# Performance work log

Measured on AMD Instinct MI355X. Metric: run time of the kernel, lower is better.

## Reference

```python
import jax, jax.numpy as jnp
import numpy as np

HID = 1024
BATCH = 32
SRC = 2048

def setup_inputs() -> dict:
    key = jax.random.key(0)
    k1, k2, k3, k4, k5 = jax.random.split(key, 5)
    hidden = jax.random.normal(k1, (BATCH, HID), dtype=jnp.float32)
    encoder_outputs = jax.random.normal(k2, (BATCH, SRC, HID), dtype=jnp.float32)
    # nn.Linear(2H, H): weight [H, 2H], bias [H]
    lim = 1.0 / np.sqrt(2 * HID)
    attn_w = jax.random.uniform(k3, (HID, 2 * HID), dtype=jnp.float32, minval=-lim, maxval=lim)
    attn_b = jax.random.uniform(k4, (HID,), dtype=jnp.float32, minval=-lim, maxval=lim)
    v = jax.random.uniform(k5, (HID,), dtype=jnp.float32)  # torch.rand
    return {"hidden": hidden, "encoder_outputs": encoder_outputs,
            "attn_w": attn_w, "attn_b": attn_b, "v": v}

def reference(hidden, encoder_outputs, attn_w, attn_b, v):
    # Split the concat linear: cat([hidden, enc]) @ W^T == hidden @ Wh^T + enc @ We^T
    w_h = attn_w[:, :HID]          # [H, H] acts on repeated hidden
    w_e = attn_w[:, HID:]          # [H, H] acts on encoder outputs
    # energy: [B, S, H]
    energy = jnp.tanh(
        jnp.einsum('bh,oh->bo', hidden, w_h)[:, None, :]
        + jnp.einsum('bsh,oh->bso', encoder_outputs, w_e)
        + attn_b
    )
    scores = jnp.einsum('bso,o->bs', energy, v)  # [B, S]
    return jax.nn.softmax(scores, axis=1)
```

## Files before the change

### kernel.cpp

```cpp
#include <hip/hip_runtime.h>
#include <hip/hip_bf16.h>

#define HID    1024
#define NBATCH 32
#define SRC    2048
#define MROWS  (NBATCH * SRC)

typedef _Float16 f16;
typedef f16   f16x8 __attribute__((ext_vector_type(8)));
typedef f16   f16x4 __attribute__((ext_vector_type(4)));
typedef float f32x4 __attribute__((ext_vector_type(4)));

#define BAR()    asm volatile("s_barrier" ::: "memory")
#define VMCNT(n) asm volatile("s_waitcnt vmcnt(" #n ")" ::: "memory")

__device__ __forceinline__ void gload_lds16(const void* g, void* l) {
  __builtin_amdgcn_global_load_lds(
      (const __attribute__((address_space(1))) void*)g,
      (__attribute__((address_space(3))) void*)l, 16, 0, 0);
}

__device__ __forceinline__ float fast_tanh(float x) {
  x = fminf(fmaxf(x, -15.f), 15.f);
  float e = __expf(2.f * x);
  return (e - 1.f) / (e + 1.f);
}

__global__ void convw_k(const float* __restrict__ attn_w, f16* __restrict__ Wf) {
  int idx = blockIdx.x * 256 + threadIdx.x;
  int j = idx * 4;
  int o = j >> 10, h = j & 1023;
  f32x4 d = *(const f32x4*)(attn_w + (size_t)o * 2048 + HID + h);
  f16x4 q = { (f16)d[0], (f16)d[1], (f16)d[2], (f16)d[3] };
  *(f16x4*)(Wf + (size_t)o * HID + h) = q;
}

__global__ void hvec_k(const float* __restrict__ hidden,
                       const float* __restrict__ attn_w,
                       const float* __restrict__ attn_b,
                       float* __restrict__ hvec) {
  int idx = blockIdx.x * 256 + threadIdx.x;
  int b = idx >> 10, o = idx & 1023;
  const float* wrow = attn_w + (size_t)o * 2048;
  const float* hrow = hidden + (size_t)b * HID;
  float acc = 0.f;
  for (int h = 0; h < HID; h += 4) {
    f32x4 wv = *(const f32x4*)(wrow + h);
    f32x4 hv = *(const f32x4*)(hrow + h);
    acc += wv[0]*hv[0] + wv[1]*hv[1] + wv[2]*hv[2] + wv[3]*hv[3];
  }
  hvec[idx] = acc + attn_b[o];
}

__global__ void convA_k(const float* __restrict__ A, f16* __restrict__ Af) {
  size_t i = ((size_t)blockIdx.x * 256 + threadIdx.x) * 8;
  f32x4 d0 = *(const f32x4*)(A + i);
  f32x4 d1 = *(const f32x4*)(A + i + 4);
  f16x8 q = { (f16)d0[0], (f16)d0[1], (f16)d0[2], (f16)d0[3],
              (f16)d1[0], (f16)d1[1], (f16)d1[2], (f16)d1[3] };
  *(f16x8*)(Af + i) = q;
}


#define STG(T) do { \
  char* la_ = lds + ((T) % 3) * 49152; char* lb_ = la_ + 32768; \
  _Pragma("unroll") for (int i_ = 0; i_ < 4; ++i_) \
    gload_lds16(Ab + (size_t)(i_ * 64 + w * 8 + sr8) * HID + (T) * 64 + scol, \
                la_ + i_ * 8192 + w * 1024); \
  _Pragma("unroll") for (int i_ = 0; i_ < 2; ++i_) \
    gload_lds16(Bb + (size_t)(i_ * 64 + w * 8 + sr8) * HID + (T) * 64 + scol, \
                lb_ + i_ * 8192 + w * 1024); } while (0)

__global__ __launch_bounds__(512, 2) void gemm_f16(
    const f16*  __restrict__ Af,
    const f16*  __restrict__ Wf,
    const float* __restrict__ hvec,
    const float* __restrict__ v,
    float* __restrict__ part)
{
  extern __shared__ __align__(16) char lds[];

  int bid = blockIdx.x;
  int wg = (bid & 7) * 256 + (bid >> 3);
  int m_idx = wg >> 3, n_idx = wg & 7;
  long row0 = (long)m_idx * 256;
  int o0 = n_idx * 128;
  int b = (int)(row0 >> 11);

  int tid = threadIdx.x;
  int l = tid & 63, w = tid >> 6;
  int wr = w >> 2, wc = w & 3;
  int lr = l & 15, lg = l >> 4;
  int sr8 = l >> 3;
  int scol = ((l & 7) ^ sr8) << 3;
  int sw = (lr & 7) << 3;

  const f16* Ab = Af + row0 * HID;
  const f16* Bb = Wf + (size_t)o0 * HID;

  f32x4 acc[8][2];
#pragma unroll
  for (int m = 0; m < 8; ++m) {
    acc[m][0] = (f32x4){0.f, 0.f, 0.f, 0.f};
    acc[m][1] = (f32x4){0.f, 0.f, 0.f, 0.f};
  }

  STG(0); STG(1);
  VMCNT(6); BAR();

  for (int T = 0; T < 16; ++T) {
    if (T + 2 < 16) STG(T + 2);
    const char* la = lds + (T % 3) * 49152;
    const char* lb = la + 32768;

    f16x8 bF[2][2];
#pragma unroll
    for (int n = 0; n < 2; ++n)
#pragma unroll
      for (int ks = 0; ks < 2; ++ks)
        bF[n][ks] = *(const f16x8*)(lb + (wc * 32 + n * 16 + lr) * 128 +
                                    (((ks * 32 + lg * 8) ^ sw) << 1));
    __builtin_amdgcn_s_setprio(1);
#pragma unroll
    for (int m = 0; m < 8; ++m) {
      const char* ra = la + (wr * 128 + m * 16 + lr) * 128;
      f16x8 a0 = *(const f16x8*)(ra + (((lg * 8) ^ sw) << 1));
      f16x8 a1 = *(const f16x8*)(ra + (((32 + lg * 8) ^ sw) << 1));
      acc[m][0] = __builtin_amdgcn_mfma_f32_16x16x32_f16(a0, bF[0][0], acc[m][0], 0, 0, 0);
      acc[m][1] = __builtin_amdgcn_mfma_f32_16x16x32_f16(a0, bF[1][0], acc[m][1], 0, 0, 0);
      acc[m][0] = __builtin_amdgcn_mfma_f32_16x16x32_f16(a1, bF[0][1], acc[m][0], 0, 0, 0);
      acc[m][1] = __builtin_amdgcn_mfma_f32_16x16x32_f16(a1, bF[1][1], acc[m][1], 0, 0, 0);
    }
    __builtin_amdgcn_s_setprio(0);

    if (T < 14)       { VMCNT(6); BAR(); }
    else if (T == 14) { VMCNT(0); BAR(); }
  }

  float hvv[2], vvv[2];
#pragma unroll
  for (int n = 0; n < 2; ++n) {
    int o = o0 + wc * 32 + n * 16 + lr;
    hvv[n] = hvec[b * HID + o];
    vvv[n] = v[o];
  }
  float* scf = (float*)lds;
  __syncthreads();
#pragma unroll
  for (int m = 0; m < 8; ++m) {
#pragma unroll
    for (int r = 0; r < 4; ++r) {
      float s = fast_tanh(acc[m][0][r] + hvv[0]) * vvv[0]
              + fast_tanh(acc[m][1][r] + hvv[1]) * vvv[1];
      s += __shfl_xor(s, 1); s += __shfl_xor(s, 2);
      s += __shfl_xor(s, 4); s += __shfl_xor(s, 8);
      if (lr == 0) scf[wc * 256 + wr * 128 + m * 16 + lg * 4 + r] = s;
    }
  }
  __syncthreads();
  if (tid < 256)
    part[(size_t)n_idx * MROWS + row0 + tid] =
        scf[tid] + scf[256 + tid] + scf[512 + tid] + scf[768 + tid];
}

__global__ __launch_bounds__(256, 2) void gemm_fb(
    const float* __restrict__ A, const f16* __restrict__ Wf,
    const float* __restrict__ hvec, const float* __restrict__ v,
    float* __restrict__ part)
{
  __shared__ __align__(16) f16 lA[128][32];
  __shared__ __align__(16) f16 lB[128][32];
  __shared__ float sc[128];

  int bid = blockIdx.x;
  int x = bid & 7, j = bid >> 3;
  int m_idx = x * 64 + (j >> 3);
  int n_idx = j & 7;
  long row0 = (long)m_idx * 128;
  int o0 = n_idx * 128;
  int b = (int)(row0 >> 11);

  int tid = threadIdx.x;
  int l = tid & 63, w = tid >> 6;
  int wr = w >> 1, wc = w & 1;
  int lr = l & 15, lg = l >> 4;

  f32x4 acc[4][4];
#pragma unroll
  for (int m = 0; m < 4; ++m)
#pragma unroll
    for (int n = 0; n < 4; ++n) acc[m][n] = (f32x4){0.f, 0.f, 0.f, 0.f};

  const float* Abase = A + row0 * 1024;

  for (int k0 = 0; k0 < 1024; k0 += 32) {
    __syncthreads();
#pragma unroll
    for (int i = 0; i < 2; ++i) {
      int rr = (i * 256 + tid) >> 2;
      const f16* src = Wf + (size_t)(o0 + rr) * HID + k0 + (tid & 3) * 8;
      char* ldsb = (char*)&lB[0][0] + i * 4096 + w * 1024;
      gload_lds16(src, ldsb);
    }
#pragma unroll
    for (int i = 0; i < 4; ++i) {
      int ja = i * 256 + tid;
      int arow = ja >> 3, ac4 = ja & 7;
      f32x4 d = *(const f32x4*)(Abase + (size_t)arow * 1024 + k0 + ac4 * 4);
      f16x4 q = { (f16)d[0], (f16)d[1], (f16)d[2], (f16)d[3] };
      *(f16x4*)&lA[arow][ac4 * 4] = q;
    }
    __syncthreads();
    f16x8 aF[4], bF[4];
#pragma unroll
    for (int m = 0; m < 4; ++m)
      aF[m] = *(const f16x8*)&lA[wr * 64 + m * 16 + lr][lg * 8];
#pragma unroll
    for (int n = 0; n < 4; ++n)
      bF[n] = *(const f16x8*)&lB[wc * 64 + n * 16 + lr][lg * 8];
#pragma unroll
    for (int m = 0; m < 4; ++m)
#pragma unroll
      for (int n = 0; n < 4; ++n)
        acc[m][n] = __builtin_amdgcn_mfma_f32_16x16x32_f16(aF[m], bF[n], acc[m][n], 0, 0, 0);
  }

  float hv[4], vv[4];
#pragma unroll
  for (int n = 0; n < 4; ++n) {
    int o = o0 + wc * 64 + n * 16 + lr;
    hv[n] = hvec[b * HID + o];
    vv[n] = v[o];
  }
  float myv[4][4];
#pragma unroll
  for (int m = 0; m < 4; ++m) {
#pragma unroll
    for (int r = 0; r < 4; ++r) {
      float s = 0.f;
#pragma unroll
      for (int n = 0; n < 4; ++n)
        s += fast_tanh(acc[m][n][r] + hv[n]) * vv[n];
      s += __shfl_xor(s, 1); s += __shfl_xor(s, 2);
      s += __shfl_xor(s, 4); s += __shfl_xor(s, 8);
      myv[m][r] = s;
    }
  }
  if (wc == 0 && lr == 0) {
#pragma unroll
    for (int m = 0; m < 4; ++m)
#pragma unroll
      for (int r = 0; r < 4; ++r)
        sc[wr * 64 + m * 16 + lg * 4 + r] = myv[m][r];
  }
  __syncthreads();
  if (wc == 1 && lr == 0) {
#pragma unroll
    for (int m = 0; m < 4; ++m)
#pragma unroll
      for (int r = 0; r < 4; ++r)
        sc[wr * 64 + m * 16 + lg * 4 + r] += myv[m][r];
  }
  __syncthreads();
  if (tid < 128)
    part[(size_t)n_idx * MROWS + row0 + tid] = sc[tid];
}

__global__ void softmax_k(const float* __restrict__ part, float* __restrict__ out) {
  int b = blockIdx.x;
  __shared__ float srow[SRC];
  __shared__ float red[8];
  int tid = threadIdx.x;

  float lmax = -1e30f;
  for (int i = tid; i < SRC; i += 256) {
    float s = 0.f;
#pragma unroll
    for (int t = 0; t < 8; ++t)
      s += part[(size_t)t * MROWS + (size_t)b * SRC + i];
    srow[i] = s;
    lmax = fmaxf(lmax, s);
  }
#pragma unroll
  for (int off = 32; off >= 1; off >>= 1)
    lmax = fmaxf(lmax, __shfl_xor(lmax, off));
  if ((tid & 63) == 0) red[tid >> 6] = lmax;
  __syncthreads();
  float bmax = fmaxf(fmaxf(red[0], red[1]), fmaxf(red[2], red[3]));

  float lsum = 0.f;
  for (int i = tid; i < SRC; i += 256) {
    float e = __expf(srow[i] - bmax);
    srow[i] = e;
    lsum += e;
  }
#pragma unroll
  for (int off = 32; off >= 1; off >>= 1)
    lsum += __shfl_xor(lsum, off);
  if ((tid & 63) == 0) red[4 + (tid >> 6)] = lsum;
  __syncthreads();
  float inv = 1.f / (red[4] + red[5] + red[6] + red[7]);
  for (int i = tid; i < SRC; i += 256)
    out[(size_t)b * SRC + i] = srow[i] * inv;
}

extern "C" void kernel_launch(void* const* d_in, const int* in_sizes, int n_in,
                              void* d_out, int out_size, void* d_ws, size_t ws_size,
                              hipStream_t stream) {
  const float* hidden = (const float*)d_in[0];
  const float* enc    = (const float*)d_in[1];
  const float* attn_w = (const float*)d_in[2];
  const float* attn_b = (const float*)d_in[3];
  const float* v      = (const float*)d_in[4];
  float* out = (float*)d_out;

  char* ws = (char*)d_ws;
  f16*   Wf   = (f16*)ws;
  float* hv   = (float*)(ws + (2ull << 20));
  float* part = (float*)(ws + (2ull << 20) + (128ull << 10));
  f16*   Af   = (f16*)(ws + (8ull << 20));

  const size_t WS_NEEDED = (8ull << 20) + (128ull << 20) + (1ull << 20);

  convw_k<<<1024, 256, 0, stream>>>(attn_w, Wf);
  hvec_k <<<128,  256, 0, stream>>>(hidden, attn_w, attn_b, hv);

  if (ws_size >= WS_NEEDED) {
    convA_k<<<32768, 256, 0, stream>>>(enc, Af);
    gemm_f16<<<2048, 512, 147456, stream>>>(Af, Wf, hv, v, part);
  } else {
    gemm_fb<<<4096, 256, 0, stream>>>(enc, Wf, hv, v, part);
  }
  softmax_k<<<NBATCH, 256, 0, stream>>>(part, out);
}
```

Before: 310.7 us.

## Widen GEMM tile to 256x256 with double-buffered phased MFMA pipeline

The fused f16 GEMM tile grows from 256x128 to 256x256 outputs per workgroup, halving the grid and the number of partial score slices (8 to 4). The main loop moves from a 3-stage ring with a per-K-step wait to a 2-buffer scheme split into four sub-phases, each interleaving two LDS-prefetch loads with MFMAs behind barriers. The goal is more reuse of each loaded A tile and less repeated A traffic. In exchange, each thread holds twice as many accumulators, which may pressure registers at 2 workgroups per CU, and there are more barriers per K step. Softmax now takes the slice count as a runtime argument.

```diff
diff --git a/kernel.cpp b/kernel.cpp
--- a/kernel.cpp
+++ b/kernel.cpp
@@ -12,7 +12,7 @@
 typedef float f32x4 __attribute__((ext_vector_type(4)));
 
 #define BAR()    asm volatile("s_barrier" ::: "memory")
-#define VMCNT(n) asm volatile("s_waitcnt vmcnt(" #n ")" ::: "memory")
+#define VMCNT0() asm volatile("s_waitcnt vmcnt(0)" ::: "memory")
 
 __device__ __forceinline__ void gload_lds16(const void* g, void* l) {
   __builtin_amdgcn_global_load_lds(
@@ -62,14 +62,41 @@
 }
 
 
-#define STG(T) do { \
-  char* la_ = lds + ((T) % 3) * 49152; char* lb_ = la_ + 32768; \
-  _Pragma("unroll") for (int i_ = 0; i_ < 4; ++i_) \
-    gload_lds16(Ab + (size_t)(i_ * 64 + w * 8 + sr8) * HID + (T) * 64 + scol, \
-                la_ + i_ * 8192 + w * 1024); \
-  _Pragma("unroll") for (int i_ = 0; i_ < 2; ++i_) \
-    gload_lds16(Bb + (size_t)(i_ * 64 + w * 8 + sr8) * HID + (T) * 64 + scol, \
-                lb_ + i_ * 8192 + w * 1024); } while (0)
+#define STG1(q, Tn, cd) do { \
+  const f16* s_ = ((q) < 4 ? Ab : Bb) + \
+      (size_t)(((q) & 3) * 64 + (tid >> 3)) * HID + (Tn) * 64 + scol; \
+  char* d_ = lds + (cd) * 65536 + ((q) < 4 ? 0 : 32768) + ((q) & 3) * 8192 + w * 1024; \
+  gload_lds16(s_, d_); } while (0)
+
+#define PHASE(P, Tn, c, DOSTG) do { \
+  const int mh_ = (P) >> 1, nh_ = (P) & 1; \
+  const char* la_ = lds + (c) * 65536; \
+  const char* lb_ = la_ + 32768; \
+  f16x8 aF[4][2], bF[2][2]; \
+  _Pragma("unroll") for (int m4 = 0; m4 < 4; ++m4) { \
+    const char* rb = la_ + (wr * 128 + mh_ * 64 + m4 * 16 + lr) * 128; \
+    aF[m4][0] = *(const f16x8*)(rb + ((lg ^ sw) << 4)); \
+    aF[m4][1] = *(const f16x8*)(rb + (((4 + lg) ^ sw) << 4)); \
+  } \
+  _Pragma("unroll") for (int n2 = 0; n2 < 2; ++n2) { \
+    const char* rb = lb_ + (wc * 64 + nh_ * 32 + n2 * 16 + lr) * 128; \
+    bF[n2][0] = *(const f16x8*)(rb + ((lg ^ sw) << 4)); \
+    bF[n2][1] = *(const f16x8*)(rb + (((4 + lg) ^ sw) << 4)); \
+  } \
+  if (DOSTG) { STG1(2 * (P), Tn, (c) ^ 1); STG1(2 * (P) + 1, Tn, (c) ^ 1); } \
+  BAR(); \
+  asm volatile("s_waitcnt lgkmcnt(0)" ::: "memory"); \
+  __builtin_amdgcn_sched_barrier(0); \
+  __builtin_amdgcn_s_setprio(1); \
+  _Pragma("unroll") for (int ks = 0; ks < 2; ++ks) \
+  _Pragma("unroll") for (int m4 = 0; m4 < 4; ++m4) \
+  _Pragma("unroll") for (int n2 = 0; n2 < 2; ++n2) \
+    acc[mh_ * 4 + m4][nh_ * 2 + n2] = __builtin_amdgcn_mfma_f32_16x16x32_f16( \
+        aF[m4][ks], bF[n2][ks], acc[mh_ * 4 + m4][nh_ * 2 + n2], 0, 0, 0); \
+  __builtin_amdgcn_s_setprio(0); \
+  if ((P) == 3 && (DOSTG)) { VMCNT0(); } \
+  BAR(); \
+} while (0)
 
 __global__ __launch_bounds__(512, 2) void gemm_f16(
     const f16*  __restrict__ Af,
@@ -81,66 +108,46 @@
   extern __shared__ __align__(16) char lds[];
 
   int bid = blockIdx.x;
-  int wg = (bid & 7) * 256 + (bid >> 3);
-  int m_idx = wg >> 3, n_idx = wg & 7;
+  int wg = (bid & 7) * 128 + (bid >> 3);
+  int m_idx = wg >> 2, n_idx = wg & 3;
   long row0 = (long)m_idx * 256;
-  int o0 = n_idx * 128;
+  int o0 = n_idx * 256;
   int b = (int)(row0 >> 11);
 
   int tid = threadIdx.x;
   int l = tid & 63, w = tid >> 6;
   int wr = w >> 2, wc = w & 3;
   int lr = l & 15, lg = l >> 4;
-  int sr8 = l >> 3;
-  int scol = ((l & 7) ^ sr8) << 3;
-  int sw = (lr & 7) << 3;
+  int sw = lr & 7;
+  int scol = ((tid & 7) ^ ((tid >> 3) & 7)) * 8;
 
   const f16* Ab = Af + row0 * HID;
   const f16* Bb = Wf + (size_t)o0 * HID;
 
-  f32x4 acc[8][2];
-#pragma unroll
-  for (int m = 0; m < 8; ++m) {
-    acc[m][0] = (f32x4){0.f, 0.f, 0.f, 0.f};
-    acc[m][1] = (f32x4){0.f, 0.f, 0.f, 0.f};
-  }
-
-  STG(0); STG(1);
-  VMCNT(6); BAR();
-
-  for (int T = 0; T < 16; ++T) {
-    if (T + 2 < 16) STG(T + 2);
-    const char* la = lds + (T % 3) * 49152;
-    const char* lb = la + 32768;
-
-    f16x8 bF[2][2];
-#pragma unroll
-    for (int n = 0; n < 2; ++n)
-#pragma unroll
-      for (int ks = 0; ks < 2; ++ks)
-        bF[n][ks] = *(const f16x8*)(lb + (wc * 32 + n * 16 + lr) * 128 +
-                                    (((ks * 32 + lg * 8) ^ sw) << 1));
-    __builtin_amdgcn_s_setprio(1);
-#pragma unroll
-    for (int m = 0; m < 8; ++m) {
-      const char* ra = la + (wr * 128 + m * 16 + lr) * 128;
-      f16x8 a0 = *(const f16x8*)(ra + (((lg * 8) ^ sw) << 1));
-      f16x8 a1 = *(const f16x8*)(ra + (((32 + lg * 8) ^ sw) << 1));
-      acc[m][0] = __builtin_amdgcn_mfma_f32_16x16x32_f16(a0, bF[0][0], acc[m][0], 0, 0, 0);
-      acc[m][1] = __builtin_amdgcn_mfma_f32_16x16x32_f16(a0, bF[1][0], acc[m][1], 0, 0, 0);
-      acc[m][0] = __builtin_amdgcn_mfma_f32_16x16x32_f16(a1, bF[0][1], acc[m][0], 0, 0, 0);
-      acc[m][1] = __builtin_amdgcn_mfma_f32_16x16x32_f16(a1, bF[1][1], acc[m][1], 0, 0, 0);
-    }
-    __builtin_amdgcn_s_setprio(0);
-
-    if (T < 14)       { VMCNT(6); BAR(); }
-    else if (T == 14) { VMCNT(0); BAR(); }
-  }
-
-  float hvv[2], vvv[2];
-#pragma unroll
-  for (int n = 0; n < 2; ++n) {
-    int o = o0 + wc * 32 + n * 16 + lr;
+  f32x4 acc[8][4];
+#pragma unroll
+  for (int m = 0; m < 8; ++m)
+#pragma unroll
+    for (int n = 0; n < 4; ++n) acc[m][n] = (f32x4){0.f, 0.f, 0.f, 0.f};
+
+#pragma unroll
+  for (int q = 0; q < 8; ++q) { STG1(q, 0, 0); }
+  VMCNT0(); BAR();
+
+#pragma unroll 1
+  for (int Tp = 0; Tp < 8; ++Tp) {
+    const int Ta = Tp * 2, Tb = Ta + 1;
+    PHASE(0, Ta + 1, 0, 1); PHASE(1, Ta + 1, 0, 1);
+    PHASE(2, Ta + 1, 0, 1); PHASE(3, Ta + 1, 0, 1);
+    const int dob = (Tb < 15);
+    PHASE(0, Tb + 1, 1, dob); PHASE(1, Tb + 1, 1, dob);
+    PHASE(2, Tb + 1, 1, dob); PHASE(3, Tb + 1, 1, dob);
+  }
+
+  float hvv[4], vvv[4];
+#pragma unroll
+  for (int n = 0; n < 4; ++n) {
+    int o = o0 + wc * 64 + n * 16 + lr;
     hvv[n] = hvec[b * HID + o];
     vvv[n] = v[o];
   }
@@ -150,8 +157,10 @@
   for (int m = 0; m < 8; ++m) {
 #pragma unroll
     for (int r = 0; r < 4; ++r) {
-      float s = fast_tanh(acc[m][0][r] + hvv[0]) * vvv[0]
-              + fast_tanh(acc[m][1][r] + hvv[1]) * vvv[1];
+      float s = 0.f;
+#pragma unroll
+      for (int n = 0; n < 4; ++n)
+        s += fast_tanh(acc[m][n][r] + hvv[n]) * vvv[n];
       s += __shfl_xor(s, 1); s += __shfl_xor(s, 2);
       s += __shfl_xor(s, 4); s += __shfl_xor(s, 8);
       if (lr == 0) scf[wc * 256 + wr * 128 + m * 16 + lg * 4 + r] = s;
@@ -266,7 +275,8 @@
     part[(size_t)n_idx * MROWS + row0 + tid] = sc[tid];
 }
 
-__global__ void softmax_k(const float* __restrict__ part, float* __restrict__ out) {
+__global__ void softmax_k(const float* __restrict__ part, float* __restrict__ out,
+                          int nsl) {
   int b = blockIdx.x;
   __shared__ float srow[SRC];
   __shared__ float red[8];
@@ -275,8 +285,7 @@
   float lmax = -1e30f;
   for (int i = tid; i < SRC; i += 256) {
     float s = 0.f;
-#pragma unroll
-    for (int t = 0; t < 8; ++t)
+    for (int t = 0; t < nsl; ++t)
       s += part[(size_t)t * MROWS + (size_t)b * SRC + i];
     srow[i] = s;
     lmax = fmaxf(lmax, s);
@@ -320,16 +329,17 @@
   float* part = (float*)(ws + (2ull << 20) + (128ull << 10));
   f16*   Af   = (f16*)(ws + (8ull << 20));
 
-  const size_t WS_NEEDED = (8ull << 20) + (128ull << 20) + (1ull << 20);
+  const size_t WS_NEEDED = (8ull << 20) + (128ull << 20);
 
   convw_k<<<1024, 256, 0, stream>>>(attn_w, Wf);
   hvec_k <<<128,  256, 0, stream>>>(hidden, attn_w, attn_b, hv);
 
   if (ws_size >= WS_NEEDED) {
     convA_k<<<32768, 256, 0, stream>>>(enc, Af);
-    gemm_f16<<<2048, 512, 147456, stream>>>(Af, Wf, hv, v, part);
+    gemm_f16<<<1024, 512, 131072, stream>>>(Af, Wf, hv, v, part);
+    softmax_k<<<NBATCH, 256, 0, stream>>>(part, out, 4);
   } else {
     gemm_fb<<<4096, 256, 0, stream>>>(enc, Wf, hv, v, part);
-  }
-  softmax_k<<<NBATCH, 256, 0, stream>>>(part, out);
-}
+    softmax_k<<<NBATCH, 256, 0, stream>>>(part, out, 8);
+  }
+}
```

Result: faster. 300.9 us (-3.2%).
